# Optimization experiments

Measured on AMD Instinct MI355X. Metric: run time of the kernel, lower is better.

The kernel has to match this reference:

```python
import jax, jax.numpy as jnp
import numpy as np

N = 100000
E = 1200000
F_IN, HID, LAT = 16, 128, 64
G = 8  # number of graphs
SG_K = 4


def setup_inputs() -> dict:
    key = jax.random.key(0)
    ks = jax.random.split(key, 20)
    x = jax.random.normal(ks[0], (N, F_IN), dtype=jnp.float32)
    edge_index = jax.random.randint(ks[1], (2, E), 0, N, dtype=jnp.int64)
    batch = jnp.sort(jax.random.randint(ks[2], (N,), 0, G, dtype=jnp.int64))

    def lin(k, fan_in, fan_out):
        s = 1.0 / np.sqrt(fan_in)
        k1, k2 = jax.random.split(k)
        W = jax.random.uniform(k1, (fan_in, fan_out), jnp.float32, -s, s)
        b = jax.random.uniform(k2, (fan_out,), jnp.float32, -s, s)
        return W, b

    W1, b1 = lin(ks[3], F_IN, HID)
    W2, b2 = lin(ks[4], HID, LAT)
    Wg1, bg1 = lin(ks[5], LAT, LAT)
    Wg2, bg2 = lin(ks[6], LAT, LAT)
    Wg3, bg3 = lin(ks[7], LAT, LAT)
    Wsg, bsg = lin(ks[8], LAT, LAT)
    Wf1, bf1 = lin(ks[9], LAT, 32)
    Wf2, bf2 = lin(ks[10], 32, 16)
    Wc, bc = lin(ks[11], 16, 1)
    Wcb, bcb = lin(ks[12], 16, 1)
    return dict(x=x, edge_index=edge_index, batch=batch,
                W1=W1, b1=b1, W2=W2, b2=b2,
                Wg1=Wg1, bg1=bg1, Wg2=Wg2, bg2=bg2, Wg3=Wg3, bg3=bg3,
                Wsg=Wsg, bsg=bsg, Wf1=Wf1, bf1=bf1, Wf2=Wf2, bf2=bf2,
                Wc=Wc, bc=bc, Wcb=Wcb, bcb=bcb)


def reference(x, edge_index, batch,
              W1, b1, W2, b2,
              Wg1, bg1, Wg2, bg2, Wg3, bg3,
              Wsg, bsg, Wf1, bf1, Wf2, bf2,
              Wc, bc, Wcb, bcb):
    n = x.shape[0]
    loops = jnp.arange(n, dtype=edge_index.dtype)
    src = jnp.concatenate([edge_index[0], loops])  # add self-loops (PyG default)
    dst = jnp.concatenate([edge_index[1], loops])
    deg = jax.ops.segment_sum(jnp.ones_like(dst, jnp.float32), dst, num_segments=n)
    dis = jnp.where(deg > 0, jax.lax.rsqrt(jnp.maximum(deg, 1.0)), 0.0)
    norm = dis[src] * dis[dst]  # symmetric GCN normalization

    def prop(h):
        # D^{-1/2} (A+I) D^{-1/2} h  via gather -> scale -> scatter-add
        return jax.ops.segment_sum(h[src] * norm[:, None], dst, num_segments=n)

    def gcn(h, W, b):
        return prop(h @ W) + b

    # encoder
    z = jax.nn.relu(gcn(x, W1, b1))
    z = gcn(z, W2, b2)
    # stacked GCNs
    z = jax.nn.relu(gcn(z, Wg1, bg1))
    z = jax.nn.relu(gcn(z, Wg2, bg2))
    z = jax.nn.relu(gcn(z, Wg3, bg3))
    # SGConv: propagate K times, then linear
    h = z
    for _ in range(SG_K):
        h = prop(h)
    z = h @ Wsg + bsg
    # global max pool per graph
    g = jax.ops.segment_max(z, batch, num_segments=G)
    g = jax.nn.relu(g @ Wf1 + bf1)
    g = jax.nn.relu(g @ Wf2 + bf2)
    cpd_pred = g @ Wc + bc
    comb_logits = g @ Wcb + bcb
    return cpd_pred, comb_logits
```

## Files before the change

kernel.cpp:

```cpp
#include <hip/hip_runtime.h>
#include <hip/hip_fp16.h>
#include <math.h>

#define G_GRAPHS 8

__device__ __forceinline__ unsigned fmap(float f) {
    unsigned b = __float_as_uint(f);
    return (b & 0x80000000u) ? ~b : (b | 0x80000000u);
}
__device__ __forceinline__ float funmap(unsigned u) {
    unsigned b = (u & 0x80000000u) ? (u & 0x7fffffffu) : ~u;
    return __uint_as_float(b);
}
__device__ __forceinline__ void fma_row(float wv, uint2 r,
                                        float& ax, float& ay, float& az, float& aw) {
    float2 f01 = __half22float2(*(__half2*)&r.x);
    float2 f23 = __half22float2(*(__half2*)&r.y);
    ax += wv * f01.x; ay += wv * f01.y; az += wv * f23.x; aw += wv * f23.y;
}
__device__ __forceinline__ uint2 pack4(float ax, float ay, float az, float aw) {
    __half2 p01 = __float22half2_rn(make_float2(ax, ay));
    __half2 p23 = __float22half2_rn(make_float2(az, aw));
    uint2 r;
    r.x = *(unsigned*)&p01;
    r.y = *(unsigned*)&p23;
    return r;
}

__global__ void k_count(const int* __restrict__ dst, int* __restrict__ deg, int E) {
    int e = blockIdx.x * 256 + threadIdx.x;
    if (e < E) atomicAdd(&deg[dst[e]], 1);
}

__global__ void k_dis(const int* __restrict__ deg, float* __restrict__ dis,
                      int* __restrict__ degp, int N) {
    int i = blockIdx.x * 256 + threadIdx.x;
    if (i < N) {
        int d = deg[i];
        dis[i] = rsqrtf((float)(d + 1));
        degp[i] = d + 1;
    }
}

__global__ void k_scanA(const int* __restrict__ deg, int* __restrict__ rowst,
                        int* __restrict__ bsum, int N) {
    __shared__ int s[256];
    int i = blockIdx.x * 256 + threadIdx.x;
    int v = (i < N) ? deg[i] + 1 : 0;
    s[threadIdx.x] = v;
    __syncthreads();
    for (int off = 1; off < 256; off <<= 1) {
        int t = (threadIdx.x >= off) ? s[threadIdx.x - off] : 0;
        __syncthreads();
        s[threadIdx.x] += t;
        __syncthreads();
    }
    if (i < N) rowst[i] = s[threadIdx.x] - v;
    if (threadIdx.x == 255) bsum[blockIdx.x] = s[255];
}

__global__ void k_scanB(int* __restrict__ bsum, int NB) {
    __shared__ int s[512];
    int t = threadIdx.x;
    int v = (t < NB) ? bsum[t] : 0;
    s[t] = v;
    __syncthreads();
    for (int off = 1; off < 512; off <<= 1) {
        int x = (t >= off) ? s[t - off] : 0;
        __syncthreads();
        s[t] += x;
        __syncthreads();
    }
    if (t < NB) bsum[t] = s[t] - v;
}

__global__ void k_scanC(int* __restrict__ rowst, const int* __restrict__ bsum, int N) {
    int i = blockIdx.x * 256 + threadIdx.x;
    if (i < N) rowst[i] += bsum[blockIdx.x];
}

__global__ void k_self(const int* __restrict__ rowst, const int* __restrict__ deg,
                       int2* __restrict__ edge, int N) {
    int i = blockIdx.x * 256 + threadIdx.x;
    if (i < N) {
        float sw = 1.0f / (float)(deg[i] + 1);
        edge[rowst[i]] = make_int2(i, __float_as_int(sw));
    }
}

__global__ void k_fill(const int* __restrict__ src, const int* __restrict__ dst,
                       const float* __restrict__ dis, const int* __restrict__ rowst,
                       int* __restrict__ cnt, int2* __restrict__ edge, int E) {
    int e = blockIdx.x * 256 + threadIdx.x;
    if (e >= E) return;
    int d = dst[e], s = src[e];
    int p = rowst[d] + 1 + atomicAdd(&cnt[d], 1);
    edge[p] = make_int2(s, __float_as_int(dis[s] * dis[d]));
}

__global__ void k_x2h(const float* __restrict__ x, __half* __restrict__ xh, int n4) {
    int i = blockIdx.x * 256 + threadIdx.x;
    if (i >= n4) return;
    float4 v = ((const float4*)x)[i];
    ((uint2*)xh)[i] = pack4(v.x, v.y, v.z, v.w);
}

__global__ __launch_bounds__(256) void k_prop16(
        const __half* __restrict__ xh, float* __restrict__ out,
        const int* __restrict__ rowst, const int* __restrict__ degp,
        const int2* __restrict__ edge, int N) {
    int t = threadIdx.x, lane = t & 63, w = t >> 6;
    int grp = lane >> 2, sub = lane & 3;
    int node = blockIdx.x * 64 + w * 16 + grp;
    if (node >= N) return;
    const uint2* xr = (const uint2*)xh;
    float ax = 0.f, ay = 0.f, az = 0.f, aw = 0.f;
    int s = rowst[node], d = degp[node];
    const int2* ep = edge + s;
    for (int i = 0; i < d; i += 4) {
        int j0 = i, j1 = i + 1, j2 = i + 2, j3 = i + 3;
        long long m0 = __builtin_nontemporal_load((const long long*)(ep + j0));
        long long m1 = __builtin_nontemporal_load((const long long*)(ep + ((j1 < d) ? j1 : 0)));
        long long m2 = __builtin_nontemporal_load((const long long*)(ep + ((j2 < d) ? j2 : 0)));
        long long m3 = __builtin_nontemporal_load((const long long*)(ep + ((j3 < d) ? j3 : 0)));
        uint2 r0 = xr[(size_t)(int)(m0 & 0xffffffffLL) * 4 + sub];
        uint2 r1 = xr[(size_t)(int)(m1 & 0xffffffffLL) * 4 + sub];
        uint2 r2 = xr[(size_t)(int)(m2 & 0xffffffffLL) * 4 + sub];
        uint2 r3 = xr[(size_t)(int)(m3 & 0xffffffffLL) * 4 + sub];
        float w0 = __int_as_float((int)(m0 >> 32));
        float w1 = (j1 < d) ? __int_as_float((int)(m1 >> 32)) : 0.f;
        float w2 = (j2 < d) ? __int_as_float((int)(m2 >> 32)) : 0.f;
        float w3 = (j3 < d) ? __int_as_float((int)(m3 >> 32)) : 0.f;
        fma_row(w0, r0, ax, ay, az, aw);
        fma_row(w1, r1, ax, ay, az, aw);
        fma_row(w2, r2, ax, ay, az, aw);
        fma_row(w3, r3, ax, ay, az, aw);
    }
    ((float4*)out)[node * 4 + sub] = make_float4(ax, ay, az, aw);
}

__global__ __launch_bounds__(256) void k_dense(
        const float* __restrict__ p0, __half* __restrict__ out,
        const float* __restrict__ W1, const float* __restrict__ b1,
        const float* __restrict__ W2, int N) {
    __shared__ float zT[4][128][4];
    int t = threadIdx.x, lane = t & 63, w = t >> 6;
    int base = (blockIdx.x * 4 + w) * 4;
    if (base >= N) return;
    float p = p0[(size_t)base * 16 + lane];
    float zA[4], zB[4];
    float bA = b1[lane], bB = b1[lane + 64];
    #pragma unroll
    for (int j = 0; j < 4; ++j) { zA[j] = bA; zB[j] = bB; }
    #pragma unroll
    for (int k = 0; k < 16; ++k) {
        float w1a = W1[k * 128 + lane];
        float w1b = W1[k * 128 + lane + 64];
        #pragma unroll
        for (int j = 0; j < 4; ++j) {
            float pk = __shfl(p, j * 16 + k);
            zA[j] += pk * w1a;
            zB[j] += pk * w1b;
        }
    }
    #pragma unroll
    for (int j = 0; j < 4; ++j) {
        zT[w][lane][j]      = fmaxf(zA[j], 0.f);
        zT[w][lane + 64][j] = fmaxf(zB[j], 0.f);
    }
    float acc[4] = {0.f, 0.f, 0.f, 0.f};
    #pragma unroll 4
    for (int k = 0; k < 128; ++k) {
        float wk = W2[k * 64 + lane];
        float4 zk = *(const float4*)&zT[w][k][0];
        acc[0] += zk.x * wk; acc[1] += zk.y * wk;
        acc[2] += zk.z * wk; acc[3] += zk.w * wk;
    }
    #pragma unroll
    for (int j = 0; j < 4; ++j)
        if (base + j < N) out[(size_t)(base + j) * 64 + lane] = __float2half(acc[j]);
}

template<bool HASW>
__global__ __launch_bounds__(256) void k_prop64(
        const __half* __restrict__ in, __half* __restrict__ out,
        const int* __restrict__ rowst, const int* __restrict__ degp,
        const int2* __restrict__ edge,
        const float* __restrict__ bias, int relu,
        const float* __restrict__ W, const float* __restrict__ gbias, int N) {
    extern __shared__ char smem[];
    unsigned* Whl = (unsigned*)smem;
    float* zb = (float*)(smem + 8192);
    int t = threadIdx.x, lane = t & 63, w = t >> 6;
    int q = lane & 15, g = lane >> 4;
    const uint2* inr = (const uint2*)in;
    if (HASW) {
        for (int i = t; i < 2048; i += 256) {
            int kk = i >> 6, l = i & 63;
            __half2 h = __floats2half2_rn(make_float2(W[(2 * kk) * 64 + l],
                                                      W[(2 * kk + 1) * 64 + l]).x,
                                          make_float2(W[(2 * kk) * 64 + l],
                                                      W[(2 * kk + 1) * 64 + l]).y);
            __half2 hh; hh.x = __float2half(W[(2 * kk) * 64 + l]);
            hh.y = __float2half(W[(2 * kk + 1) * 64 + l]);
            Whl[i] = *(unsigned*)&hh;
        }
        __syncthreads();
    }
    float4 b4 = make_float4(0.f, 0.f, 0.f, 0.f);
    if (bias) b4 = ((const float4*)bias)[q];
    float gb = (HASW && gbias) ? gbias[lane] : 0.f;
    int wid = blockIdx.x * 4 + w;
    const int stride = gridDim.x * 4 * 2;
    for (int n0 = wid * 2; n0 < N; n0 += stride) {
        int n1 = n0 + 1;
        bool h1 = n1 < N;
        int s0 = rowst[n0], d0 = degp[n0];
        int s1 = h1 ? rowst[n1] : s0, d1 = h1 ? degp[n1] : 0;
        const int2* e0 = edge + s0;
        const int2* e1 = edge + s1;
        float a0x = 0.f, a0y = 0.f, a0z = 0.f, a0w = 0.f;
        float a1x = 0.f, a1y = 0.f, a1z = 0.f, a1w = 0.f;
        int m = d0 > d1 ? d0 : d1;
        for (int base = 0; base < m; base += 16) {
            int i0 = base + g, i1 = i0 + 4, i2 = i0 + 8, i3 = i0 + 12;
            long long ma0 = __builtin_nontemporal_load((const long long*)(e0 + ((i0 < d0) ? i0 : 0)));
            long long ma1 = __builtin_nontemporal_load((const long long*)(e0 + ((i1 < d0) ? i1 : 0)));
            long long ma2 = __builtin_nontemporal_load((const long long*)(e0 + ((i2 < d0) ? i2 : 0)));
            long long ma3 = __builtin_nontemporal_load((const long long*)(e0 + ((i3 < d0) ? i3 : 0)));
            long long mb0 = __builtin_nontemporal_load((const long long*)(e1 + ((i0 < d1) ? i0 : 0)));
            long long mb1 = __builtin_nontemporal_load((const long long*)(e1 + ((i1 < d1) ? i1 : 0)));
            long long mb2 = __builtin_nontemporal_load((const long long*)(e1 + ((i2 < d1) ? i2 : 0)));
            long long mb3 = __builtin_nontemporal_load((const long long*)(e1 + ((i3 < d1) ? i3 : 0)));
            uint2 ra0 = inr[(size_t)(int)(ma0 & 0xffffffffLL) * 16 + q];
            uint2 ra1 = inr[(size_t)(int)(ma1 & 0xffffffffLL) * 16 + q];
            uint2 ra2 = inr[(size_t)(int)(ma2 & 0xffffffffLL) * 16 + q];
            uint2 ra3 = inr[(size_t)(int)(ma3 & 0xffffffffLL) * 16 + q];
            uint2 rb0 = inr[(size_t)(int)(mb0 & 0xffffffffLL) * 16 + q];
            uint2 rb1 = inr[(size_t)(int)(mb1 & 0xffffffffLL) * 16 + q];
            uint2 rb2 = inr[(size_t)(int)(mb2 & 0xffffffffLL) * 16 + q];
            uint2 rb3 = inr[(size_t)(int)(mb3 & 0xffffffffLL) * 16 + q];
            float wa0 = (i0 < d0) ? __int_as_float((int)(ma0 >> 32)) : 0.f;
            float wa1 = (i1 < d0) ? __int_as_float((int)(ma1 >> 32)) : 0.f;
            float wa2 = (i2 < d0) ? __int_as_float((int)(ma2 >> 32)) : 0.f;
            float wa3 = (i3 < d0) ? __int_as_float((int)(ma3 >> 32)) : 0.f;
            float wb0 = (i0 < d1) ? __int_as_float((int)(mb0 >> 32)) : 0.f;
            float wb1 = (i1 < d1) ? __int_as_float((int)(mb1 >> 32)) : 0.f;
            float wb2 = (i2 < d1) ? __int_as_float((int)(mb2 >> 32)) : 0.f;
            float wb3 = (i3 < d1) ? __int_as_float((int)(mb3 >> 32)) : 0.f;
            fma_row(wa0, ra0, a0x, a0y, a0z, a0w);
            fma_row(wa1, ra1, a0x, a0y, a0z, a0w);
            fma_row(wa2, ra2, a0x, a0y, a0z, a0w);
            fma_row(wa3, ra3, a0x, a0y, a0z, a0w);
            fma_row(wb0, rb0, a1x, a1y, a1z, a1w);
            fma_row(wb1, rb1, a1x, a1y, a1z, a1w);
            fma_row(wb2, rb2, a1x, a1y, a1z, a1w);
            fma_row(wb3, rb3, a1x, a1y, a1z, a1w);
        }
        a0x += __shfl_xor(a0x,16); a0y += __shfl_xor(a0y,16); a0z += __shfl_xor(a0z,16); a0w += __shfl_xor(a0w,16);
        a0x += __shfl_xor(a0x,32); a0y += __shfl_xor(a0y,32); a0z += __shfl_xor(a0z,32); a0w += __shfl_xor(a0w,32);
        a1x += __shfl_xor(a1x,16); a1y += __shfl_xor(a1y,16); a1z += __shfl_xor(a1z,16); a1w += __shfl_xor(a1w,16);
        a1x += __shfl_xor(a1x,32); a1y += __shfl_xor(a1y,32); a1z += __shfl_xor(a1z,32); a1w += __shfl_xor(a1w,32);
        a0x += b4.x; a0y += b4.y; a0z += b4.z; a0w += b4.w;
        a1x += b4.x; a1y += b4.y; a1z += b4.z; a1w += b4.w;
        if (relu) {
            a0x = fmaxf(a0x,0.f); a0y = fmaxf(a0y,0.f); a0z = fmaxf(a0z,0.f); a0w = fmaxf(a0w,0.f);
            a1x = fmaxf(a1x,0.f); a1y = fmaxf(a1y,0.f); a1z = fmaxf(a1z,0.f); a1w = fmaxf(a1w,0.f);
        }
        if (!HASW) {
            if (g == 0) {
                ((uint2*)out)[(size_t)n0 * 16 + q] = pack4(a0x, a0y, a0z, a0w);
                if (h1) ((uint2*)out)[(size_t)n1 * 16 + q] = pack4(a1x, a1y, a1z, a1w);
            }
        } else {
            if (g == 0) {
                ((float4*)&zb[(w * 2 + 0) * 64])[q] = make_float4(a0x, a0y, a0z, a0w);
                ((float4*)&zb[(w * 2 + 1) * 64])[q] = make_float4(a1x, a1y, a1z, a1w);
            }
            float acc0 = gb, acc1 = gb;
            #pragma unroll 8
            for (int kk = 0; kk < 32; ++kk) {
                unsigned u = Whl[kk * 64 + lane];
                float2 wp = __half22float2(*(__half2*)&u);
                float2 z0 = *(float2*)&zb[(w * 2 + 0) * 64 + 2 * kk];
                float2 z1 = *(float2*)&zb[(w * 2 + 1) * 64 + 2 * kk];
                acc0 += z0.x * wp.x + z0.y * wp.y;
                acc1 += z1.x * wp.x + z1.y * wp.y;
            }
            out[(size_t)n0 * 64 + lane] = __float2half(acc0);
            if (h1) out[(size_t)n1 * 64 + lane] = __float2half(acc1);
        }
    }
}

__global__ void k_pool_init(unsigned* __restrict__ gmax) {
    gmax[blockIdx.x * 64 + threadIdx.x] = fmap(-INFINITY);
}

__global__ void k_pool(const __half* __restrict__ z, const int* __restrict__ batch,
                       unsigned* __restrict__ gmax, int N) {
    int f = threadIdx.x & 63, w = threadIdx.x >> 6;
    int base = (blockIdx.x * 4 + w) * 32;
    if (base >= N) return;
    int end = base + 32; if (end > N) end = N;
    int b0 = batch[base], b1 = batch[end - 1];
    if (b0 == b1) {
        float lmax = -INFINITY;
        for (int n = base; n < end; ++n)
            lmax = fmaxf(lmax, __half2float(z[(size_t)n * 64 + f]));
        atomicMax(&gmax[b0 * 64 + f], fmap(lmax));
    } else {
        int curb = b0; float lmax = -INFINITY;
        for (int n = base; n < end; ++n) {
            int b = batch[n];
            if (b != curb) {
                atomicMax(&gmax[curb * 64 + f], fmap(lmax));
                curb = b; lmax = -INFINITY;
            }
            lmax = fmaxf(lmax, __half2float(z[(size_t)n * 64 + f]));
        }
        atomicMax(&gmax[curb * 64 + f], fmap(lmax));
    }
}

__global__ void k_head(const unsigned* __restrict__ gmax,
                       const float* __restrict__ Wf1, const float* __restrict__ bf1,
                       const float* __restrict__ Wf2, const float* __restrict__ bf2,
                       const float* __restrict__ Wc, const float* __restrict__ bc,
                       const float* __restrict__ Wcb, const float* __restrict__ bcb,
                       float* __restrict__ out) {
    __shared__ float g[8][64], h1[8][32], h2[8][16];
    int t = threadIdx.x;
    for (int i = t; i < 512; i += 64) g[i >> 6][i & 63] = funmap(gmax[i]);
    __syncthreads();
    for (int i = t; i < 256; i += 64) {
        int r = i >> 5, c = i & 31;
        float a = bf1[c];
        for (int k = 0; k < 64; ++k) a += g[r][k] * Wf1[k * 32 + c];
        h1[r][c] = fmaxf(a, 0.f);
    }
    __syncthreads();
    for (int i = t; i < 128; i += 64) {
        int r = i >> 4, c = i & 15;
        float a = bf2[c];
        for (int k = 0; k < 32; ++k) a += h1[r][k] * Wf2[k * 16 + c];
        h2[r][c] = fmaxf(a, 0.f);
    }
    __syncthreads();
    if (t < 16) {
        int r = t & 7;
        bool comb = t >= 8;
        const float* W = comb ? Wcb : Wc;
        float a = comb ? bcb[0] : bc[0];
        for (int k = 0; k < 16; ++k) a += h2[r][k] * W[k];
        out[(comb ? 8 : 0) + r] = a;
    }
}

extern "C" void kernel_launch(void* const* d_in, const int* in_sizes, int n_in,
                              void* d_out, int out_size, void* d_ws, size_t ws_size,
                              hipStream_t stream) {
    const float* x    = (const float*)d_in[0];
    const int*   ei   = (const int*)d_in[1];
    const int*   batch= (const int*)d_in[2];
    const float* W1   = (const float*)d_in[3];
    const float* b1   = (const float*)d_in[4];
    const float* W2   = (const float*)d_in[5];
    const float* b2   = (const float*)d_in[6];
    const float* Wg1  = (const float*)d_in[7];
    const float* bg1  = (const float*)d_in[8];
    const float* Wg2  = (const float*)d_in[9];
    const float* bg2  = (const float*)d_in[10];
    const float* Wg3  = (const float*)d_in[11];
    const float* bg3  = (const float*)d_in[12];
    const float* Wsg  = (const float*)d_in[13];
    const float* bsg  = (const float*)d_in[14];
    const float* Wf1  = (const float*)d_in[15];
    const float* bf1  = (const float*)d_in[16];
    const float* Wf2  = (const float*)d_in[17];
    const float* bf2  = (const float*)d_in[18];
    const float* Wc   = (const float*)d_in[19];
    const float* bc   = (const float*)d_in[20];
    const float* Wcb  = (const float*)d_in[21];
    const float* bcb  = (const float*)d_in[22];

    const int N = in_sizes[0] / 16;
    const int E = in_sizes[1] / 2;
    const int* esrc = ei;
    const int* edst = ei + E;

    char* ws = (char*)d_ws;
    auto alloc = [&](size_t bytes) -> char* {
        char* p = ws;
        ws += (bytes + 255) & ~(size_t)255;
        return p;
    };
    int*      deg   = (int*)alloc((size_t)N * 4);
    int*      degp  = (int*)alloc((size_t)N * 4);
    int*      cnt   = (int*)alloc((size_t)N * 4);
    int*      rowst = (int*)alloc((size_t)(N + 1) * 4);
    int*      bsum  = (int*)alloc(4096);
    float*    dis   = (float*)alloc((size_t)N * 4);
    int2*     edge  = (int2*)alloc((size_t)(E + N + 16) * 8);
    __half*   xh    = (__half*)alloc((size_t)N * 16 * 2);
    float*    p0    = (float*)alloc((size_t)N * 16 * 4);
    __half*   bufA  = (__half*)alloc((size_t)N * 64 * 2);
    __half*   bufB  = (__half*)alloc((size_t)N * 64 * 2);
    unsigned* gmax  = (unsigned*)alloc((size_t)G_GRAPHS * 64 * 4);

    hipMemsetAsync(deg, 0, (size_t)N * 4, stream);
    hipMemsetAsync(cnt, 0, (size_t)N * 4, stream);

    const int EB = (E + 255) / 256;
    const int NB = (N + 255) / 256;
    const int PB = 2048;
    const size_t SW = 10240;

    k_count<<<EB, 256, 0, stream>>>(edst, deg, E);
    k_dis<<<NB, 256, 0, stream>>>(deg, dis, degp, N);
    k_scanA<<<NB, 256, 0, stream>>>(deg, rowst, bsum, N);
    k_scanB<<<1, 512, 0, stream>>>(bsum, NB);
    k_scanC<<<NB, 256, 0, stream>>>(rowst, bsum, N);
    k_self<<<NB, 256, 0, stream>>>(rowst, deg, edge, N);
    k_fill<<<EB, 256, 0, stream>>>(esrc, edst, dis, rowst, cnt, edge, E);
    k_x2h<<<(N * 4 + 255) / 256, 256, 0, stream>>>(x, xh, N * 4);

    k_prop16<<<(N + 63) / 64, 256, 0, stream>>>(xh, p0, rowst, degp, edge, N);
    k_dense<<<(N + 15) / 16, 256, 0, stream>>>(p0, bufA, W1, b1, W2, N);
    k_prop64<true><<<PB, 256, SW, stream>>>(bufA, bufB, rowst, degp, edge, b2, 0, Wg1, nullptr, N);
    k_prop64<true><<<PB, 256, SW, stream>>>(bufB, bufA, rowst, degp, edge, bg1, 1, Wg2, nullptr, N);
    k_prop64<true><<<PB, 256, SW, stream>>>(bufA, bufB, rowst, degp, edge, bg2, 1, Wg3, nullptr, N);
    k_prop64<false><<<PB, 256, 0, stream>>>(bufB, bufA, rowst, degp, edge, bg3, 1, nullptr, nullptr, N);
    k_prop64<false><<<PB, 256, 0, stream>>>(bufA, bufB, rowst, degp, edge, nullptr, 0, nullptr, nullptr, N);
    k_prop64<false><<<PB, 256, 0, stream>>>(bufB, bufA, rowst, degp, edge, nullptr, 0, nullptr, nullptr, N);
    k_prop64<false><<<PB, 256, 0, stream>>>(bufA, bufB, rowst, degp, edge, nullptr, 0, nullptr, nullptr, N);
    k_prop64<true><<<PB, 256, SW, stream>>>(bufB, bufA, rowst, degp, edge, nullptr, 0, Wsg, bsg, N);

    k_pool_init<<<G_GRAPHS, 64, 0, stream>>>(gmax);
    k_pool<<<(N + 127) / 128, 256, 0, stream>>>(bufA, batch, gmax, N);
    k_head<<<1, 64, 0, stream>>>(gmax, Wf1, bf1, Wf2, bf2, Wc, bc, Wcb, bcb, (float*)d_out);
}
```

Measured before the change: 672.1 us.

## Handle self-loops in-kernel, widen prop64 lanes to 8 halves, drop nontemporal loads

```diff
diff --git a/kernel.cpp b/kernel.cpp
--- a/kernel.cpp
+++ b/kernel.cpp
@@ -12,11 +12,21 @@
     unsigned b = (u & 0x80000000u) ? (u & 0x7fffffffu) : ~u;
     return __uint_as_float(b);
 }
-__device__ __forceinline__ void fma_row(float wv, uint2 r,
-                                        float& ax, float& ay, float& az, float& aw) {
+__device__ __forceinline__ void fma_row4(float wv, uint2 r,
+                                         float& ax, float& ay, float& az, float& aw) {
     float2 f01 = __half22float2(*(__half2*)&r.x);
     float2 f23 = __half22float2(*(__half2*)&r.y);
     ax += wv * f01.x; ay += wv * f01.y; az += wv * f23.x; aw += wv * f23.y;
+}
+__device__ __forceinline__ void fma_row8(float wv, uint4 r, float* a) {
+    float2 f0 = __half22float2(*(__half2*)&r.x);
+    float2 f1 = __half22float2(*(__half2*)&r.y);
+    float2 f2 = __half22float2(*(__half2*)&r.z);
+    float2 f3 = __half22float2(*(__half2*)&r.w);
+    a[0] += wv * f0.x; a[1] += wv * f0.y;
+    a[2] += wv * f1.x; a[3] += wv * f1.y;
+    a[4] += wv * f2.x; a[5] += wv * f2.y;
+    a[6] += wv * f3.x; a[7] += wv * f3.y;
 }
 __device__ __forceinline__ uint2 pack4(float ax, float ay, float az, float aw) {
     __half2 p01 = __float22half2_rn(make_float2(ax, ay));
@@ -26,27 +36,32 @@
     r.y = *(unsigned*)&p23;
     return r;
 }
+__device__ __forceinline__ uint4 pack8(const float* a) {
+    __half2 h0 = __float22half2_rn(make_float2(a[0], a[1]));
+    __half2 h1 = __float22half2_rn(make_float2(a[2], a[3]));
+    __half2 h2 = __float22half2_rn(make_float2(a[4], a[5]));
+    __half2 h3 = __float22half2_rn(make_float2(a[6], a[7]));
+    uint4 r;
+    r.x = *(unsigned*)&h0; r.y = *(unsigned*)&h1;
+    r.z = *(unsigned*)&h2; r.w = *(unsigned*)&h3;
+    return r;
+}
 
 __global__ void k_count(const int* __restrict__ dst, int* __restrict__ deg, int E) {
     int e = blockIdx.x * 256 + threadIdx.x;
     if (e < E) atomicAdd(&deg[dst[e]], 1);
 }
 
-__global__ void k_dis(const int* __restrict__ deg, float* __restrict__ dis,
-                      int* __restrict__ degp, int N) {
+__global__ void k_dis(const int* __restrict__ deg, float* __restrict__ dis, int N) {
     int i = blockIdx.x * 256 + threadIdx.x;
-    if (i < N) {
-        int d = deg[i];
-        dis[i] = rsqrtf((float)(d + 1));
-        degp[i] = d + 1;
-    }
+    if (i < N) dis[i] = rsqrtf((float)(deg[i] + 1));
 }
 
 __global__ void k_scanA(const int* __restrict__ deg, int* __restrict__ rowst,
                         int* __restrict__ bsum, int N) {
     __shared__ int s[256];
     int i = blockIdx.x * 256 + threadIdx.x;
-    int v = (i < N) ? deg[i] + 1 : 0;
+    int v = (i < N) ? deg[i] : 0;
     s[threadIdx.x] = v;
     __syncthreads();
     for (int off = 1; off < 256; off <<= 1) {
@@ -79,22 +94,13 @@
     if (i < N) rowst[i] += bsum[blockIdx.x];
 }
 
-__global__ void k_self(const int* __restrict__ rowst, const int* __restrict__ deg,
-                       int2* __restrict__ edge, int N) {
-    int i = blockIdx.x * 256 + threadIdx.x;
-    if (i < N) {
-        float sw = 1.0f / (float)(deg[i] + 1);
-        edge[rowst[i]] = make_int2(i, __float_as_int(sw));
-    }
-}
-
 __global__ void k_fill(const int* __restrict__ src, const int* __restrict__ dst,
                        const float* __restrict__ dis, const int* __restrict__ rowst,
                        int* __restrict__ cnt, int2* __restrict__ edge, int E) {
     int e = blockIdx.x * 256 + threadIdx.x;
     if (e >= E) return;
     int d = dst[e], s = src[e];
-    int p = rowst[d] + 1 + atomicAdd(&cnt[d], 1);
+    int p = rowst[d] + atomicAdd(&cnt[d], 1);
     edge[p] = make_int2(s, __float_as_int(dis[s] * dis[d]));
 }
 
@@ -107,36 +113,38 @@
 
 __global__ __launch_bounds__(256) void k_prop16(
         const __half* __restrict__ xh, float* __restrict__ out,
-        const int* __restrict__ rowst, const int* __restrict__ degp,
+        const int* __restrict__ rowst, const int* __restrict__ deg,
         const int2* __restrict__ edge, int N) {
     int t = threadIdx.x, lane = t & 63, w = t >> 6;
     int grp = lane >> 2, sub = lane & 3;
     int node = blockIdx.x * 64 + w * 16 + grp;
     if (node >= N) return;
     const uint2* xr = (const uint2*)xh;
+    int s = rowst[node], d = deg[node];
+    float sc = 1.0f / (float)(d + 1);
     float ax = 0.f, ay = 0.f, az = 0.f, aw = 0.f;
-    int s = rowst[node], d = degp[node];
+    fma_row4(sc, xr[(size_t)node * 4 + sub], ax, ay, az, aw);
     const int2* ep = edge + s;
     for (int i = 0; i < d; i += 4) {
-        int j0 = i, j1 = i + 1, j2 = i + 2, j3 = i + 3;
-        long long m0 = __builtin_nontemporal_load((const long long*)(ep + j0));
-        long long m1 = __builtin_nontemporal_load((const long long*)(ep + ((j1 < d) ? j1 : 0)));
-        long long m2 = __builtin_nontemporal_load((const long long*)(ep + ((j2 < d) ? j2 : 0)));
-        long long m3 = __builtin_nontemporal_load((const long long*)(ep + ((j3 < d) ? j3 : 0)));
-        uint2 r0 = xr[(size_t)(int)(m0 & 0xffffffffLL) * 4 + sub];
-        uint2 r1 = xr[(size_t)(int)(m1 & 0xffffffffLL) * 4 + sub];
-        uint2 r2 = xr[(size_t)(int)(m2 & 0xffffffffLL) * 4 + sub];
-        uint2 r3 = xr[(size_t)(int)(m3 & 0xffffffffLL) * 4 + sub];
-        float w0 = __int_as_float((int)(m0 >> 32));
-        float w1 = (j1 < d) ? __int_as_float((int)(m1 >> 32)) : 0.f;
-        float w2 = (j2 < d) ? __int_as_float((int)(m2 >> 32)) : 0.f;
-        float w3 = (j3 < d) ? __int_as_float((int)(m3 >> 32)) : 0.f;
-        fma_row(w0, r0, ax, ay, az, aw);
-        fma_row(w1, r1, ax, ay, az, aw);
-        fma_row(w2, r2, ax, ay, az, aw);
-        fma_row(w3, r3, ax, ay, az, aw);
-    }
-    ((float4*)out)[node * 4 + sub] = make_float4(ax, ay, az, aw);
+        int j1 = i + 1, j2 = i + 2, j3 = i + 3;
+        int2 e0 = ep[i];
+        int2 e1 = ep[(j1 < d) ? j1 : 0];
+        int2 e2 = ep[(j2 < d) ? j2 : 0];
+        int2 e3 = ep[(j3 < d) ? j3 : 0];
+        uint2 r0 = xr[(size_t)e0.x * 4 + sub];
+        uint2 r1 = xr[(size_t)e1.x * 4 + sub];
+        uint2 r2 = xr[(size_t)e2.x * 4 + sub];
+        uint2 r3 = xr[(size_t)e3.x * 4 + sub];
+        float w0 = __int_as_float(e0.y);
+        float w1 = (j1 < d) ? __int_as_float(e1.y) : 0.f;
+        float w2 = (j2 < d) ? __int_as_float(e2.y) : 0.f;
+        float w3 = (j3 < d) ? __int_as_float(e3.y) : 0.f;
+        fma_row4(w0, r0, ax, ay, az, aw);
+        fma_row4(w1, r1, ax, ay, az, aw);
+        fma_row4(w2, r2, ax, ay, az, aw);
+        fma_row4(w3, r3, ax, ay, az, aw);
+    }
+    ((float4*)out)[(size_t)node * 4 + sub] = make_float4(ax, ay, az, aw);
 }
 
 __global__ __launch_bounds__(256) void k_dense(
@@ -184,7 +192,7 @@
 template<bool HASW>
 __global__ __launch_bounds__(256) void k_prop64(
         const __half* __restrict__ in, __half* __restrict__ out,
-        const int* __restrict__ rowst, const int* __restrict__ degp,
+        const int* __restrict__ rowst, const int* __restrict__ deg,
         const int2* __restrict__ edge,
         const float* __restrict__ bias, int relu,
         const float* __restrict__ W, const float* __restrict__ gbias, int N) {
@@ -192,90 +200,100 @@
     unsigned* Whl = (unsigned*)smem;
     float* zb = (float*)(smem + 8192);
     int t = threadIdx.x, lane = t & 63, w = t >> 6;
-    int q = lane & 15, g = lane >> 4;
-    const uint2* inr = (const uint2*)in;
+    int q = lane & 7, g = lane >> 3;
+    const uint4* inr = (const uint4*)in;
     if (HASW) {
         for (int i = t; i < 2048; i += 256) {
             int kk = i >> 6, l = i & 63;
-            __half2 h = __floats2half2_rn(make_float2(W[(2 * kk) * 64 + l],
-                                                      W[(2 * kk + 1) * 64 + l]).x,
-                                          make_float2(W[(2 * kk) * 64 + l],
-                                                      W[(2 * kk + 1) * 64 + l]).y);
-            __half2 hh; hh.x = __float2half(W[(2 * kk) * 64 + l]);
+            __half2 hh;
+            hh.x = __float2half(W[(2 * kk) * 64 + l]);
             hh.y = __float2half(W[(2 * kk + 1) * 64 + l]);
             Whl[i] = *(unsigned*)&hh;
         }
         __syncthreads();
     }
-    float4 b4 = make_float4(0.f, 0.f, 0.f, 0.f);
-    if (bias) b4 = ((const float4*)bias)[q];
+    float b8[8] = {0.f, 0.f, 0.f, 0.f, 0.f, 0.f, 0.f, 0.f};
+    if (bias) {
+        float4 t0 = ((const float4*)bias)[q * 2];
+        float4 t1 = ((const float4*)bias)[q * 2 + 1];
+        b8[0] = t0.x; b8[1] = t0.y; b8[2] = t0.z; b8[3] = t0.w;
+        b8[4] = t1.x; b8[5] = t1.y; b8[6] = t1.z; b8[7] = t1.w;
+    }
     float gb = (HASW && gbias) ? gbias[lane] : 0.f;
     int wid = blockIdx.x * 4 + w;
     const int stride = gridDim.x * 4 * 2;
     for (int n0 = wid * 2; n0 < N; n0 += stride) {
         int n1 = n0 + 1;
         bool h1 = n1 < N;
-        int s0 = rowst[n0], d0 = degp[n0];
-        int s1 = h1 ? rowst[n1] : s0, d1 = h1 ? degp[n1] : 0;
+        int s0 = rowst[n0], d0 = deg[n0];
+        int s1 = h1 ? rowst[n1] : s0, d1 = h1 ? deg[n1] : 0;
         const int2* e0 = edge + s0;
         const int2* e1 = edge + s1;
-        float a0x = 0.f, a0y = 0.f, a0z = 0.f, a0w = 0.f;
-        float a1x = 0.f, a1y = 0.f, a1z = 0.f, a1w = 0.f;
+        float a0[8] = {0,0,0,0,0,0,0,0};
+        float a1[8] = {0,0,0,0,0,0,0,0};
+        fma_row8(0.125f / (float)(d0 + 1), inr[(size_t)n0 * 8 + q], a0);
+        fma_row8(h1 ? 0.125f / (float)(d1 + 1) : 0.f,
+                 inr[(size_t)(h1 ? n1 : n0) * 8 + q], a1);
         int m = d0 > d1 ? d0 : d1;
         for (int base = 0; base < m; base += 16) {
-            int i0 = base + g, i1 = i0 + 4, i2 = i0 + 8, i3 = i0 + 12;
-            long long ma0 = __builtin_nontemporal_load((const long long*)(e0 + ((i0 < d0) ? i0 : 0)));
-            long long ma1 = __builtin_nontemporal_load((const long long*)(e0 + ((i1 < d0) ? i1 : 0)));
-            long long ma2 = __builtin_nontemporal_load((const long long*)(e0 + ((i2 < d0) ? i2 : 0)));
-            long long ma3 = __builtin_nontemporal_load((const long long*)(e0 + ((i3 < d0) ? i3 : 0)));
-            long long mb0 = __builtin_nontemporal_load((const long long*)(e1 + ((i0 < d1) ? i0 : 0)));
-            long long mb1 = __builtin_nontemporal_load((const long long*)(e1 + ((i1 < d1) ? i1 : 0)));
-            long long mb2 = __builtin_nontemporal_load((const long long*)(e1 + ((i2 < d1) ? i2 : 0)));
-            long long mb3 = __builtin_nontemporal_load((const long long*)(e1 + ((i3 < d1) ? i3 : 0)));
-            uint2 ra0 = inr[(size_t)(int)(ma0 & 0xffffffffLL) * 16 + q];
-            uint2 ra1 = inr[(size_t)(int)(ma1 & 0xffffffffLL) * 16 + q];
-            uint2 ra2 = inr[(size_t)(int)(ma2 & 0xffffffffLL) * 16 + q];
-            uint2 ra3 = inr[(size_t)(int)(ma3 & 0xffffffffLL) * 16 + q];
-            uint2 rb0 = inr[(size_t)(int)(mb0 & 0xffffffffLL) * 16 + q];
-            uint2 rb1 = inr[(size_t)(int)(mb1 & 0xffffffffLL) * 16 + q];
-            uint2 rb2 = inr[(size_t)(int)(mb2 & 0xffffffffLL) * 16 + q];
-            uint2 rb3 = inr[(size_t)(int)(mb3 & 0xffffffffLL) * 16 + q];
-            float wa0 = (i0 < d0) ? __int_as_float((int)(ma0 >> 32)) : 0.f;
-            float wa1 = (i1 < d0) ? __int_as_float((int)(ma1 >> 32)) : 0.f;
-            float wa2 = (i2 < d0) ? __int_as_float((int)(ma2 >> 32)) : 0.f;
-            float wa3 = (i3 < d0) ? __int_as_float((int)(ma3 >> 32)) : 0.f;
-            float wb0 = (i0 < d1) ? __int_as_float((int)(mb0 >> 32)) : 0.f;
-            float wb1 = (i1 < d1) ? __int_as_float((int)(mb1 >> 32)) : 0.f;
-            float wb2 = (i2 < d1) ? __int_as_float((int)(mb2 >> 32)) : 0.f;
-            float wb3 = (i3 < d1) ? __int_as_float((int)(mb3 >> 32)) : 0.f;
-            fma_row(wa0, ra0, a0x, a0y, a0z, a0w);
-            fma_row(wa1, ra1, a0x, a0y, a0z, a0w);
-            fma_row(wa2, ra2, a0x, a0y, a0z, a0w);
-            fma_row(wa3, ra3, a0x, a0y, a0z, a0w);
-            fma_row(wb0, rb0, a1x, a1y, a1z, a1w);
-            fma_row(wb1, rb1, a1x, a1y, a1z, a1w);
-            fma_row(wb2, rb2, a1x, a1y, a1z, a1w);
-            fma_row(wb3, rb3, a1x, a1y, a1z, a1w);
-        }
-        a0x += __shfl_xor(a0x,16); a0y += __shfl_xor(a0y,16); a0z += __shfl_xor(a0z,16); a0w += __shfl_xor(a0w,16);
-        a0x += __shfl_xor(a0x,32); a0y += __shfl_xor(a0y,32); a0z += __shfl_xor(a0z,32); a0w += __shfl_xor(a0w,32);
-        a1x += __shfl_xor(a1x,16); a1y += __shfl_xor(a1y,16); a1z += __shfl_xor(a1z,16); a1w += __shfl_xor(a1w,16);
-        a1x += __shfl_xor(a1x,32); a1y += __shfl_xor(a1y,32); a1z += __shfl_xor(a1z,32); a1w += __shfl_xor(a1w,32);
-        a0x += b4.x; a0y += b4.y; a0z += b4.z; a0w += b4.w;
-        a1x += b4.x; a1y += b4.y; a1z += b4.z; a1w += b4.w;
+            int i0 = base + g, i1 = base + g + 8;
+            int2 ma0 = e0[(i0 < d0) ? i0 : 0];
+            int2 ma1 = e0[(i1 < d0) ? i1 : 0];
+            int2 mb0 = e1[(i0 < d1) ? i0 : 0];
+            int2 mb1 = e1[(i1 < d1) ? i1 : 0];
+            uint4 ra0 = inr[(size_t)ma0.x * 8 + q];
+            uint4 ra1 = inr[(size_t)ma1.x * 8 + q];
+            uint4 rb0 = inr[(size_t)mb0.x * 8 + q];
+            uint4 rb1 = inr[(size_t)mb1.x * 8 + q];
+            float wa0 = (i0 < d0) ? __int_as_float(ma0.y) : 0.f;
+            float wa1 = (i1 < d0) ? __int_as_float(ma1.y) : 0.f;
+            float wb0 = (i0 < d1) ? __int_as_float(mb0.y) : 0.f;
+            float wb1 = (i1 < d1) ? __int_as_float(mb1.y) : 0.f;
+            fma_row8(wa0, ra0, a0);
+            fma_row8(wa1, ra1, a0);
+            fma_row8(wb0, rb0, a1);
+            fma_row8(wb1, rb1, a1);
+        }
+        #pragma unroll
+        for (int j = 0; j < 8; ++j) {
+            a0[j] += __shfl_xor(a0[j], 8);
+            a1[j] += __shfl_xor(a1[j], 8);
+        }
+        #pragma unroll
+        for (int j = 0; j < 8; ++j) {
+            a0[j] += __shfl_xor(a0[j], 16);
+            a1[j] += __shfl_xor(a1[j], 16);
+        }
+        #pragma unroll
+        for (int j = 0; j < 8; ++j) {
+            a0[j] += __shfl_xor(a0[j], 32);
+            a1[j] += __shfl_xor(a1[j], 32);
+        }
+        #pragma unroll
+        for (int j = 0; j < 8; ++j) {
+            a0[j] += b8[j];
+            a1[j] += b8[j];
+        }
         if (relu) {
-            a0x = fmaxf(a0x,0.f); a0y = fmaxf(a0y,0.f); a0z = fmaxf(a0z,0.f); a0w = fmaxf(a0w,0.f);
-            a1x = fmaxf(a1x,0.f); a1y = fmaxf(a1y,0.f); a1z = fmaxf(a1z,0.f); a1w = fmaxf(a1w,0.f);
+            #pragma unroll
+            for (int j = 0; j < 8; ++j) {
+                a0[j] = fmaxf(a0[j], 0.f);
+                a1[j] = fmaxf(a1[j], 0.f);
+            }
         }
         if (!HASW) {
             if (g == 0) {
-                ((uint2*)out)[(size_t)n0 * 16 + q] = pack4(a0x, a0y, a0z, a0w);
-                if (h1) ((uint2*)out)[(size_t)n1 * 16 + q] = pack4(a1x, a1y, a1z, a1w);
+                ((uint4*)out)[(size_t)n0 * 8 + q] = pack8(a0);
+                if (h1) ((uint4*)out)[(size_t)n1 * 8 + q] = pack8(a1);
             }
         } else {
             if (g == 0) {
-                ((float4*)&zb[(w * 2 + 0) * 64])[q] = make_float4(a0x, a0y, a0z, a0w);
-                ((float4*)&zb[(w * 2 + 1) * 64])[q] = make_float4(a1x, a1y, a1z, a1w);
+                float* z0 = &zb[(w * 2 + 0) * 64 + q * 8];
+                float* z1 = &zb[(w * 2 + 1) * 64 + q * 8];
+                *(float4*)&z0[0] = make_float4(a0[0], a0[1], a0[2], a0[3]);
+                *(float4*)&z0[4] = make_float4(a0[4], a0[5], a0[6], a0[7]);
+                *(float4*)&z1[0] = make_float4(a1[0], a1[1], a1[2], a1[3]);
+                *(float4*)&z1[4] = make_float4(a1[4], a1[5], a1[6], a1[7]);
             }
             float acc0 = gb, acc1 = gb;
             #pragma unroll 8
@@ -396,12 +414,11 @@
         return p;
     };
     int*      deg   = (int*)alloc((size_t)N * 4);
-    int*      degp  = (int*)alloc((size_t)N * 4);
     int*      cnt   = (int*)alloc((size_t)N * 4);
     int*      rowst = (int*)alloc((size_t)(N + 1) * 4);
     int*      bsum  = (int*)alloc(4096);
     float*    dis   = (float*)alloc((size_t)N * 4);
-    int2*     edge  = (int2*)alloc((size_t)(E + N + 16) * 8);
+    int2*     edge  = (int2*)alloc((size_t)(E + 16) * 8);
     __half*   xh    = (__half*)alloc((size_t)N * 16 * 2);
     float*    p0    = (float*)alloc((size_t)N * 16 * 4);
     __half*   bufA  = (__half*)alloc((size_t)N * 64 * 2);
@@ -410,6 +427,7 @@
 
     hipMemsetAsync(deg, 0, (size_t)N * 4, stream);
     hipMemsetAsync(cnt, 0, (size_t)N * 4, stream);
+    hipMemsetAsync(edge + E, 0, 16 * 8, stream);
 
     const int EB = (E + 255) / 256;
     const int NB = (N + 255) / 256;
@@ -417,24 +435,23 @@
     const size_t SW = 10240;
 
     k_count<<<EB, 256, 0, stream>>>(edst, deg, E);
-    k_dis<<<NB, 256, 0, stream>>>(deg, dis, degp, N);
+    k_dis<<<NB, 256, 0, stream>>>(deg, dis, N);
     k_scanA<<<NB, 256, 0, stream>>>(deg, rowst, bsum, N);
     k_scanB<<<1, 512, 0, stream>>>(bsum, NB);
     k_scanC<<<NB, 256, 0, stream>>>(rowst, bsum, N);
-    k_self<<<NB, 256, 0, stream>>>(rowst, deg, edge, N);
     k_fill<<<EB, 256, 0, stream>>>(esrc, edst, dis, rowst, cnt, edge, E);
     k_x2h<<<(N * 4 + 255) / 256, 256, 0, stream>>>(x, xh, N * 4);
 
-    k_prop16<<<(N + 63) / 64, 256, 0, stream>>>(xh, p0, rowst, degp, edge, N);
+    k_prop16<<<(N + 63) / 64, 256, 0, stream>>>(xh, p0, rowst, deg, edge, N);
     k_dense<<<(N + 15) / 16, 256, 0, stream>>>(p0, bufA, W1, b1, W2, N);
-    k_prop64<true><<<PB, 256, SW, stream>>>(bufA, bufB, rowst, degp, edge, b2, 0, Wg1, nullptr, N);
-    k_prop64<true><<<PB, 256, SW, stream>>>(bufB, bufA, rowst, degp, edge, bg1, 1, Wg2, nullptr, N);
-    k_prop64<true><<<PB, 256, SW, stream>>>(bufA, bufB, rowst, degp, edge, bg2, 1, Wg3, nullptr, N);
-    k_prop64<false><<<PB, 256, 0, stream>>>(bufB, bufA, rowst, degp, edge, bg3, 1, nullptr, nullptr, N);
-    k_prop64<false><<<PB, 256, 0, stream>>>(bufA, bufB, rowst, degp, edge, nullptr, 0, nullptr, nullptr, N);
-    k_prop64<false><<<PB, 256, 0, stream>>>(bufB, bufA, rowst, degp, edge, nullptr, 0, nullptr, nullptr, N);
-    k_prop64<false><<<PB, 256, 0, stream>>>(bufA, bufB, rowst, degp, edge, nullptr, 0, nullptr, nullptr, N);
-    k_prop64<true><<<PB, 256, SW, stream>>>(bufB, bufA, rowst, degp, edge, nullptr, 0, Wsg, bsg, N);
+    k_prop64<true><<<PB, 256, SW, stream>>>(bufA, bufB, rowst, deg, edge, b2, 0, Wg1, nullptr, N);
+    k_prop64<true><<<PB, 256, SW, stream>>>(bufB, bufA, rowst, deg, edge, bg1, 1, Wg2, nullptr, N);
+    k_prop64<true><<<PB, 256, SW, stream>>>(bufA, bufB, rowst, deg, edge, bg2, 1, Wg3, nullptr, N);
+    k_prop64<false><<<PB, 256, 0, stream>>>(bufB, bufA, rowst, deg, edge, bg3, 1, nullptr, nullptr, N);
+    k_prop64<false><<<PB, 256, 0, stream>>>(bufA, bufB, rowst, deg, edge, nullptr, 0, nullptr, nullptr, N);
+    k_prop64<false><<<PB, 256, 0, stream>>>(bufB, bufA, rowst, deg, edge, nullptr, 0, nullptr, nullptr, N);
+    k_prop64<false><<<PB, 256, 0, stream>>>(bufA, bufB, rowst, deg, edge, nullptr, 0, nullptr, nullptr, N);
+    k_prop64<true><<<PB, 256, SW, stream>>>(bufB, bufA, rowst, deg, edge, nullptr, 0, Wsg, bsg, N);
 
     k_pool_init<<<G_GRAPHS, 64, 0, stream>>>(gmax);
     k_pool<<<(N + 127) / 128, 256, 0, stream>>>(bufA, batch, gmax, N);
```

Result: no change. 662.7 us (-1.4%).
